# Kernel optimization log

Measured on AMD Instinct MI355X. Metric: run time of the kernel, lower is better.

Reference implementation:

```python
import jax, jax.numpy as jnp
import numpy as np

B, S, D, H = 4, 2048, 1024, 16
DK = D // H
FF = 2 * D


def _layer_norm(x, g, b, eps):
    mu = jnp.mean(x, axis=-1, keepdims=True)
    var = jnp.mean(jnp.square(x - mu), axis=-1, keepdims=True)
    return (x - mu) * jax.lax.rsqrt(var + eps) * g + b


def setup_inputs() -> dict:
    key = jax.random.key(0)
    ks = jax.random.split(key, 8)
    s = 1.0 / np.sqrt(D)
    return {
        "x": jax.random.normal(ks[0], (B, S, D), jnp.float32),
        "Wq": jax.random.normal(ks[1], (D, D), jnp.float32) * s,
        "Wk": jax.random.normal(ks[2], (D, D), jnp.float32) * s,
        "Wv": jax.random.normal(ks[3], (D, D), jnp.float32) * s,
        "Wo": jax.random.normal(ks[4], (D, D), jnp.float32) * s,
        "ln1_g": jnp.ones((D,), jnp.float32),
        "ln1_b": jnp.zeros((D,), jnp.float32),
        "fc1_w": jax.random.normal(ks[5], (D, FF), jnp.float32) * s,
        "fc1_b": jnp.zeros((FF,), jnp.float32),
        "fc2_w": jax.random.normal(ks[6], (FF, D), jnp.float32) * (1.0 / np.sqrt(FF)),
        "fc2_b": jnp.zeros((D,), jnp.float32),
        "ln2_g": jnp.ones((D,), jnp.float32),
        "ln2_b": jnp.zeros((D,), jnp.float32),
    }


def reference(x, Wq, Wk, Wv, Wo, ln1_g, ln1_b, fc1_w, fc1_b, fc2_w, fc2_b, ln2_g, ln2_b):
    # --- multi-head self-attention (pre-LN, residual) ---
    residual = x
    xn = _layer_norm(x, ln1_g, ln1_b, 1e-5)  # nn.LayerNorm default eps
    q = (xn @ Wq).reshape(B, S, H, DK)
    k = (xn @ Wk).reshape(B, S, H, DK)
    v = (xn @ Wv).reshape(B, S, H, DK)
    scores = jnp.einsum("bqhd,bkhd->bhqk", q, k) / jnp.sqrt(jnp.float32(DK))
    attn = jax.nn.softmax(scores, axis=-1)  # dropout p=0.0 -> identity
    out = jnp.einsum("bhqk,bkhd->bqhd", attn, v).reshape(B, S, D)
    out = out @ Wo + residual
    # --- residual feed-forward (pre-LN, eps=1e-6) ---
    h = _layer_norm(out, ln2_g, ln2_b, 1e-6)
    h = jax.nn.relu(h @ fc1_w + fc1_b)
    h = h @ fc2_w + fc2_b
    return out + h
```

## Files before the change

kernel.cpp:

```cpp
#include <hip/hip_runtime.h>

#define BB   4
#define SS   2048
#define DDIM 1024
#define HH   16
#define DKK  64
#define FFF  2048
#define NTOK (BB * SS)

typedef __bf16 bf16x8 __attribute__((ext_vector_type(8)));
typedef float floatx4 __attribute__((ext_vector_type(4)));

__device__ __forceinline__ unsigned short f2bf(float f) {
    union { float f; unsigned u; } v; v.f = f;
    unsigned r = v.u + 0x7fffu + ((v.u >> 16) & 1u);
    return (unsigned short)(r >> 16);
}

__device__ __forceinline__ void async_copy16(const unsigned short* g, unsigned short* l) {
    __builtin_amdgcn_global_load_lds(
        (const __attribute__((address_space(1))) void*)g,
        (__attribute__((address_space(3))) void*)l, 16, 0, 0);
}

__device__ __forceinline__ unsigned pack_bf_trunc(float a, float b) {
    union { float f; unsigned u; } x, y; x.f = a; y.f = b;
    return __builtin_amdgcn_perm(y.u, x.u, 0x07060302u);
}

__global__ __launch_bounds__(256) void transpose_all(
    const float* __restrict__ Wq, const float* __restrict__ Wk,
    const float* __restrict__ Wv, const float* __restrict__ Wo,
    const float* __restrict__ fc1, const float* __restrict__ fc2,
    unsigned short* __restrict__ wqkT, unsigned short* __restrict__ wvT,
    unsigned short* __restrict__ woT, unsigned short* __restrict__ fc1T,
    unsigned short* __restrict__ fc2T) {
    __shared__ float tile[64][65];
    int t = blockIdx.x;
    const float* src; unsigned short* dst; int K, N, tl;
    if (t < 256)       { src = Wq;  dst = wqkT;                       K = 1024; N = 1024; tl = t; }
    else if (t < 512)  { src = Wk;  dst = wqkT + (size_t)1024 * 1024; K = 1024; N = 1024; tl = t - 256; }
    else if (t < 768)  { src = Wv;  dst = wvT;                        K = 1024; N = 1024; tl = t - 512; }
    else if (t < 1024) { src = Wo;  dst = woT;                        K = 1024; N = 1024; tl = t - 768; }
    else if (t < 1536) { src = fc1; dst = fc1T;                       K = 1024; N = 2048; tl = t - 1024; }
    else               { src = fc2; dst = fc2T;                       K = 2048; N = 1024; tl = t - 1536; }
    int kt = K >> 6;
    int k0 = (tl & (kt - 1)) * 64, n0 = (tl / kt) * 64;
    int tid = threadIdx.x;
#pragma unroll
    for (int i = 0; i < 16; ++i) {
        int e = i * 256 + tid;
        int r = e >> 6, c = e & 63;
        tile[r][c] = src[(size_t)(k0 + r) * N + (n0 + c)];
    }
    __syncthreads();
#pragma unroll
    for (int i = 0; i < 16; ++i) {
        int e = i * 256 + tid;
        int r = e >> 6, c = e & 63;
        dst[(size_t)(n0 + r) * K + (k0 + c)] = f2bf(tile[c][r]);
    }
}

__device__ __forceinline__ float block_sum256(float s) {
#pragma unroll
    for (int o = 32; o > 0; o >>= 1) s += __shfl_xor(s, o);
    __shared__ float partial[4];
    int w = threadIdx.x >> 6;
    __syncthreads();
    if ((threadIdx.x & 63) == 0) partial[w] = s;
    __syncthreads();
    return partial[0] + partial[1] + partial[2] + partial[3];
}

__global__ __launch_bounds__(256) void layernorm_bf16(
    const float* __restrict__ x, const float* __restrict__ g,
    const float* __restrict__ b, unsigned short* __restrict__ out, float eps) {
    size_t row = blockIdx.x;
    const float* xr = x + row * DDIM;
    int tid = threadIdx.x;
    float4 v = *(const float4*)(xr + tid * 4);
    float mu = block_sum256(v.x + v.y + v.z + v.w) * (1.0f / DDIM);
    float dx = v.x - mu, dy = v.y - mu, dz = v.z - mu, dw = v.w - mu;
    float var = block_sum256(dx * dx + dy * dy + dz * dz + dw * dw) * (1.0f / DDIM);
    float rstd = rsqrtf(var + eps);
    int c = tid * 4;
    unsigned short* o = out + row * DDIM + c;
    o[0] = f2bf(dx * rstd * g[c + 0] + b[c + 0]);
    o[1] = f2bf(dy * rstd * g[c + 1] + b[c + 1]);
    o[2] = f2bf(dz * rstd * g[c + 2] + b[c + 2]);
    o[3] = f2bf(dw * rstd * g[c + 3] + b[c + 3]);
}

__global__ __launch_bounds__(256) void gemm_bt128(
    const unsigned short* __restrict__ A, const unsigned short* __restrict__ Bt,
    const float* __restrict__ bias, const float* __restrict__ resid,
    float* __restrict__ outf, unsigned short* __restrict__ outh,
    int M, int N, int K, int relu) {
    __shared__ unsigned short As[128 * 64];
    __shared__ unsigned short Bs[128 * 64];
    int tid = threadIdx.x;
    int wave = tid >> 6, lane = tid & 63;
    int lr = lane & 15, quad = lane >> 4;
    int bid = blockIdx.x;
    int m0 = (bid & 63) * 128;
    int n0 = (bid >> 6) * 128;
    int wm = (wave >> 1) * 64, wn = (wave & 1) * 64;

    floatx4 acc[4][4];
#pragma unroll
    for (int i = 0; i < 4; ++i)
#pragma unroll
        for (int t = 0; t < 4; ++t)
#pragma unroll
            for (int r = 0; r < 4; ++r) acc[i][t][r] = 0.0f;

    int srow = 32 * wave + (lane >> 3);
    int scol = (lane & 7) * 8;
    const unsigned short* ag[4];
    const unsigned short* bg[4];
    unsigned short* al[4];
    unsigned short* bl[4];
#pragma unroll
    for (int c = 0; c < 4; ++c) {
        ag[c] = A  + (size_t)(m0 + srow + 8 * c) * K + scol;
        bg[c] = Bt + (size_t)(n0 + srow + 8 * c) * K + scol;
        al[c] = &As[(32 * wave + 8 * c) * 64];
        bl[c] = &Bs[(32 * wave + 8 * c) * 64];
    }

    for (int k0 = 0; k0 < K; k0 += 64) {
#pragma unroll
        for (int c = 0; c < 4; ++c) {
            async_copy16(ag[c] + k0, al[c]);
            async_copy16(bg[c] + k0, bl[c]);
        }
        __syncthreads();
#pragma unroll
        for (int kk = 0; kk < 2; ++kk) {
            bf16x8 af[4], bfr[4];
#pragma unroll
            for (int i = 0; i < 4; ++i)
                af[i] = *(const bf16x8*)&As[(wm + 16 * i + lr) * 64 + kk * 32 + quad * 8];
#pragma unroll
            for (int t = 0; t < 4; ++t)
                bfr[t] = *(const bf16x8*)&Bs[(wn + 16 * t + lr) * 64 + kk * 32 + quad * 8];
#pragma unroll
            for (int i = 0; i < 4; ++i)
#pragma unroll
                for (int t = 0; t < 4; ++t)
                    acc[i][t] = __builtin_amdgcn_mfma_f32_16x16x32_bf16(af[i], bfr[t], acc[i][t], 0, 0, 0);
        }
        __syncthreads();
    }

#pragma unroll
    for (int i = 0; i < 4; ++i) {
#pragma unroll
        for (int t = 0; t < 4; ++t) {
            int col = n0 + wn + 16 * t + lr;
#pragma unroll
            for (int r = 0; r < 4; ++r) {
                int row = m0 + wm + 16 * i + quad * 4 + r;
                float v = acc[i][t][r];
                if (bias)  v += bias[col];
                if (resid) v += resid[(size_t)row * N + col];
                if (relu)  v = fmaxf(v, 0.0f);
                size_t idx = (size_t)row * N + col;
                if (outf) outf[idx] = v;
                else      outh[idx] = f2bf(v);
            }
        }
    }
}

__global__ __launch_bounds__(256) void transpose_v(
    const unsigned short* __restrict__ vb, unsigned short* __restrict__ vt) {
    int bh = blockIdx.y;
    int b = bh >> 4, h = bh & 15;
    int s = blockIdx.x * 256 + threadIdx.x;
    size_t inbase = ((size_t)(b * SS + s)) * DDIM + h * 64;
    size_t outbase = (size_t)bh * 64 * SS;
    int sp = (s & ~63) + 4 * (s & 15) + ((s >> 4) & 3);
#pragma unroll
    for (int dk8 = 0; dk8 < 8; ++dk8) {
        uint4 raw = *(const uint4*)(vb + inbase + dk8 * 8);
        const unsigned short* ph = (const unsigned short*)&raw;
#pragma unroll
        for (int i = 0; i < 8; ++i)
            vt[outbase + (size_t)(dk8 * 8 + i) * SS + sp] = ph[i];
    }
}

#define AST 72
#define VST 136

__global__ __launch_bounds__(256, 2) void attention_mfma4(
    const unsigned short* __restrict__ qk, const unsigned short* __restrict__ vt,
    unsigned short* __restrict__ ctx) {
    __shared__ unsigned short Qs[128 * AST];
    __shared__ unsigned short Ks[128 * AST];
    __shared__ unsigned short Vs[64 * VST];
    __shared__ unsigned short Ps[128 * AST];

    int tid = threadIdx.x;
    int wave = tid >> 6, lane = tid & 63;
    int lr = lane & 15, quad = lane >> 4;

    int bid = blockIdx.x;
    int bh = bid & 63;
    int qt = bid >> 6;
    int b = bh >> 4, h = bh & 15;
    int q0 = qt * 128;
    size_t q_base = ((size_t)b * SS) * 2048 + h * 64;
    size_t k_base = q_base + 1024;
    size_t vt_base = (size_t)bh * 64 * SS;

#pragma unroll
    for (int i = 0; i < 4; ++i) {
        int e = i * 256 + tid;
        int r = e >> 3, c8 = (e & 7) * 8;
        *(uint4*)&Qs[r * AST + c8] =
            *(const uint4*)(qk + q_base + (size_t)(q0 + r) * 2048 + c8);
    }

    floatx4 o[2][4];
    float l[2][4];
#pragma unroll
    for (int g = 0; g < 2; ++g)
#pragma unroll
        for (int t = 0; t < 4; ++t)
#pragma unroll
            for (int r = 0; r < 4; ++r) o[g][t][r] = 0.0f;
#pragma unroll
    for (int g = 0; g < 2; ++g)
#pragma unroll
        for (int r = 0; r < 4; ++r) l[g][r] = 0.0f;

    const float C = 0.18033688011112042f;

    for (int jt = 0; jt < SS / 128; ++jt) {
#pragma unroll
        for (int i = 0; i < 4; ++i) {
            int e = i * 256 + tid;
            int r = e >> 3, c8 = (e & 7) * 8;
            *(uint4*)&Ks[r * AST + c8] =
                *(const uint4*)(qk + k_base + (size_t)(jt * 128 + r) * 2048 + c8);
        }
#pragma unroll
        for (int i = 0; i < 4; ++i) {
            int e = i * 256 + tid;
            int r = e >> 4, c8 = (e & 15) * 8;
            *(uint4*)&Vs[r * VST + c8] =
                *(const uint4*)(vt + vt_base + (size_t)r * SS + jt * 128 + c8);
        }
        __syncthreads();

        floatx4 s[2][8];
#pragma unroll
        for (int g = 0; g < 2; ++g)
#pragma unroll
            for (int t = 0; t < 8; ++t)
#pragma unroll
                for (int r = 0; r < 4; ++r) s[g][t][r] = 0.0f;
#pragma unroll
        for (int kk = 0; kk < 2; ++kk) {
            bf16x8 af0 = *(const bf16x8*)&Qs[(32 * wave + lr) * AST + kk * 32 + quad * 8];
            bf16x8 af1 = *(const bf16x8*)&Qs[(32 * wave + 16 + lr) * AST + kk * 32 + quad * 8];
#pragma unroll
            for (int t = 0; t < 8; ++t) {
                bf16x8 bfr = *(const bf16x8*)&Ks[(16 * t + lr) * AST + kk * 32 + quad * 8];
                s[0][t] = __builtin_amdgcn_mfma_f32_16x16x32_bf16(af0, bfr, s[0][t], 0, 0, 0);
                s[1][t] = __builtin_amdgcn_mfma_f32_16x16x32_bf16(af1, bfr, s[1][t], 0, 0, 0);
            }
        }

        uint2 pw1[2][4];
#pragma unroll
        for (int g = 0; g < 2; ++g) {
#pragma unroll
            for (int r = 0; r < 4; ++r) {
                float p[8];
#pragma unroll
                for (int t = 0; t < 8; ++t) p[t] = exp2f(s[g][t][r] * C);
                l[g][r] += ((p[0] + p[1]) + (p[2] + p[3])) + ((p[4] + p[5]) + (p[6] + p[7]));
                uint2 w0;
                w0.x = pack_bf_trunc(p[0], p[1]);
                w0.y = pack_bf_trunc(p[2], p[3]);
                *(uint2*)&Ps[(32 * wave + 16 * g + quad * 4 + r) * AST + 4 * lr] = w0;
                pw1[g][r].x = pack_bf_trunc(p[4], p[5]);
                pw1[g][r].y = pack_bf_trunc(p[6], p[7]);
            }
        }

#pragma unroll
        for (int kk = 0; kk < 2; ++kk) {
            bf16x8 pf0 = *(const bf16x8*)&Ps[(32 * wave + lr) * AST + kk * 32 + quad * 8];
            bf16x8 pf1 = *(const bf16x8*)&Ps[(32 * wave + 16 + lr) * AST + kk * 32 + quad * 8];
#pragma unroll
            for (int t = 0; t < 4; ++t) {
                bf16x8 vf = *(const bf16x8*)&Vs[(16 * t + lr) * VST + kk * 32 + quad * 8];
                o[0][t] = __builtin_amdgcn_mfma_f32_16x16x32_bf16(pf0, vf, o[0][t], 0, 0, 0);
                o[1][t] = __builtin_amdgcn_mfma_f32_16x16x32_bf16(pf1, vf, o[1][t], 0, 0, 0);
            }
        }
#pragma unroll
        for (int g = 0; g < 2; ++g)
#pragma unroll
            for (int r = 0; r < 4; ++r)
                *(uint2*)&Ps[(32 * wave + 16 * g + quad * 4 + r) * AST + 4 * lr] = pw1[g][r];
#pragma unroll
        for (int kk = 0; kk < 2; ++kk) {
            bf16x8 pf0 = *(const bf16x8*)&Ps[(32 * wave + lr) * AST + kk * 32 + quad * 8];
            bf16x8 pf1 = *(const bf16x8*)&Ps[(32 * wave + 16 + lr) * AST + kk * 32 + quad * 8];
#pragma unroll
            for (int t = 0; t < 4; ++t) {
                bf16x8 vf = *(const bf16x8*)&Vs[(16 * t + lr) * VST + 64 + kk * 32 + quad * 8];
                o[0][t] = __builtin_amdgcn_mfma_f32_16x16x32_bf16(pf0, vf, o[0][t], 0, 0, 0);
                o[1][t] = __builtin_amdgcn_mfma_f32_16x16x32_bf16(pf1, vf, o[1][t], 0, 0, 0);
            }
        }
        __syncthreads();
    }

#pragma unroll
    for (int g = 0; g < 2; ++g) {
#pragma unroll
        for (int r = 0; r < 4; ++r) {
            float ls = l[g][r];
            ls += __shfl_xor(ls, 1);
            ls += __shfl_xor(ls, 2);
            ls += __shfl_xor(ls, 4);
            ls += __shfl_xor(ls, 8);
            float inv = 1.0f / ls;
            int row = q0 + 32 * wave + 16 * g + quad * 4 + r;
            size_t base = ((size_t)(b * SS + row)) * DDIM + h * 64;
#pragma unroll
            for (int t = 0; t < 4; ++t)
                ctx[base + 16 * t + lr] = f2bf(o[g][t][r] * inv);
        }
    }
}

extern "C" void kernel_launch(void* const* d_in, const int* in_sizes, int n_in,
                              void* d_out, int out_size, void* d_ws, size_t ws_size,
                              hipStream_t stream) {
    const float* x     = (const float*)d_in[0];
    const float* Wq    = (const float*)d_in[1];
    const float* Wk    = (const float*)d_in[2];
    const float* Wv    = (const float*)d_in[3];
    const float* Wo    = (const float*)d_in[4];
    const float* ln1g  = (const float*)d_in[5];
    const float* ln1b  = (const float*)d_in[6];
    const float* fc1w  = (const float*)d_in[7];
    const float* fc1b  = (const float*)d_in[8];
    const float* fc2w  = (const float*)d_in[9];
    const float* fc2b  = (const float*)d_in[10];
    const float* ln2g  = (const float*)d_in[11];
    const float* ln2b  = (const float*)d_in[12];
    float* out = (float*)d_out;

    char* ws = (char*)d_ws;
    const size_t MB = 1024 * 1024;
    unsigned short* wqkT = (unsigned short*)(ws + 0 * MB);
    unsigned short* wvT  = (unsigned short*)(ws + 4 * MB);
    unsigned short* woT  = (unsigned short*)(ws + 6 * MB);
    unsigned short* fc1T = (unsigned short*)(ws + 8 * MB);
    unsigned short* fc2T = (unsigned short*)(ws + 12 * MB);
    unsigned short* xn   = (unsigned short*)(ws + 16 * MB);
    unsigned short* vt   = xn;
    unsigned short* hn   = xn;
    unsigned short* qkb  = (unsigned short*)(ws + 32 * MB);
    unsigned short* h1   = qkb;
    unsigned short* vb   = (unsigned short*)(ws + 64 * MB);
    unsigned short* ctx  = vb;

    dim3 blk(256);

    transpose_all<<<2048, blk, 0, stream>>>(Wq, Wk, Wv, Wo, fc1w, fc2w,
                                            wqkT, wvT, woT, fc1T, fc2T);

    layernorm_bf16<<<NTOK, blk, 0, stream>>>(x, ln1g, ln1b, xn, 1e-5f);

    gemm_bt128<<<1024, blk, 0, stream>>>(xn, wqkT, nullptr, nullptr, nullptr, qkb, NTOK, 2048, 1024, 0);
    gemm_bt128<<<512, blk, 0, stream>>>(xn, wvT, nullptr, nullptr, nullptr, vb, NTOK, 1024, 1024, 0);
    transpose_v<<<dim3(8, 64), blk, 0, stream>>>(vb, vt);

    attention_mfma4<<<1024, blk, 0, stream>>>(qkb, vt, ctx);

    gemm_bt128<<<512, blk, 0, stream>>>(ctx, woT, nullptr, x, out, nullptr, NTOK, 1024, 1024, 0);
    layernorm_bf16<<<NTOK, blk, 0, stream>>>(out, ln2g, ln2b, hn, 1e-6f);
    gemm_bt128<<<1024, blk, 0, stream>>>(hn, fc1T, fc1b, nullptr, nullptr, h1, NTOK, 2048, 1024, 1);
    gemm_bt128<<<512, blk, 0, stream>>>(h1, fc2T, fc2b, out, out, nullptr, NTOK, 1024, 2048, 0);
}
```

Measured before the change: 579.8 us.

## Load MFMA fragments directly from global memory in GEMM and attention

The GEMM drops LDS staging and async copies: each wave loads its A/B MFMA fragments straight from global memory into registers, with no block barriers. Attention is restructured so waves split the key range in two halves, keep Q fragments in registers, and read K and transposed V directly from global memory. Partial outputs and row sums are combined through LDS at the end. This removes LDS traffic and syncs, but gives up cross-wave reuse inside a block, so it relies on cache hits and adds more global load instructions.

```diff
diff --git a/kernel.cpp b/kernel.cpp
--- a/kernel.cpp
+++ b/kernel.cpp
@@ -17,15 +17,13 @@
     return (unsigned short)(r >> 16);
 }
 
-__device__ __forceinline__ void async_copy16(const unsigned short* g, unsigned short* l) {
-    __builtin_amdgcn_global_load_lds(
-        (const __attribute__((address_space(1))) void*)g,
-        (__attribute__((address_space(3))) void*)l, 16, 0, 0);
-}
-
 __device__ __forceinline__ unsigned pack_bf_trunc(float a, float b) {
     union { float f; unsigned u; } x, y; x.f = a; y.f = b;
     return __builtin_amdgcn_perm(y.u, x.u, 0x07060302u);
+}
+
+__device__ __forceinline__ bf16x8 as_frag(uint4 v) {
+    union { uint4 u; bf16x8 f; } c; c.u = v; return c.f;
 }
 
 __global__ __launch_bounds__(256) void transpose_all(
@@ -92,13 +90,11 @@
     o[3] = f2bf(dw * rstd * g[c + 3] + b[c + 3]);
 }
 
-__global__ __launch_bounds__(256) void gemm_bt128(
+__global__ __launch_bounds__(256, 2) void gemm_reg(
     const unsigned short* __restrict__ A, const unsigned short* __restrict__ Bt,
     const float* __restrict__ bias, const float* __restrict__ resid,
     float* __restrict__ outf, unsigned short* __restrict__ outh,
     int M, int N, int K, int relu) {
-    __shared__ unsigned short As[128 * 64];
-    __shared__ unsigned short Bs[128 * 64];
     int tid = threadIdx.x;
     int wave = tid >> 6, lane = tid & 63;
     int lr = lane & 15, quad = lane >> 4;
@@ -115,43 +111,22 @@
 #pragma unroll
             for (int r = 0; r < 4; ++r) acc[i][t][r] = 0.0f;
 
-    int srow = 32 * wave + (lane >> 3);
-    int scol = (lane & 7) * 8;
-    const unsigned short* ag[4];
-    const unsigned short* bg[4];
-    unsigned short* al[4];
-    unsigned short* bl[4];
-#pragma unroll
-    for (int c = 0; c < 4; ++c) {
-        ag[c] = A  + (size_t)(m0 + srow + 8 * c) * K + scol;
-        bg[c] = Bt + (size_t)(n0 + srow + 8 * c) * K + scol;
-        al[c] = &As[(32 * wave + 8 * c) * 64];
-        bl[c] = &Bs[(32 * wave + 8 * c) * 64];
-    }
-
-    for (int k0 = 0; k0 < K; k0 += 64) {
-#pragma unroll
-        for (int c = 0; c < 4; ++c) {
-            async_copy16(ag[c] + k0, al[c]);
-            async_copy16(bg[c] + k0, bl[c]);
-        }
-        __syncthreads();
-#pragma unroll
-        for (int kk = 0; kk < 2; ++kk) {
-            bf16x8 af[4], bfr[4];
-#pragma unroll
-            for (int i = 0; i < 4; ++i)
-                af[i] = *(const bf16x8*)&As[(wm + 16 * i + lr) * 64 + kk * 32 + quad * 8];
+    const unsigned short* ap = A  + (size_t)(m0 + wm + lr) * K + quad * 8;
+    const unsigned short* bp = Bt + (size_t)(n0 + wn + lr) * K + quad * 8;
+
+    for (int k0 = 0; k0 < K; k0 += 32) {
+        uint4 av[4], bv[4];
+#pragma unroll
+        for (int i = 0; i < 4; ++i) {
+            av[i] = *(const uint4*)(ap + (size_t)(16 * i) * K + k0);
+            bv[i] = *(const uint4*)(bp + (size_t)(16 * i) * K + k0);
+        }
+#pragma unroll
+        for (int i = 0; i < 4; ++i)
 #pragma unroll
             for (int t = 0; t < 4; ++t)
-                bfr[t] = *(const bf16x8*)&Bs[(wn + 16 * t + lr) * 64 + kk * 32 + quad * 8];
-#pragma unroll
-            for (int i = 0; i < 4; ++i)
-#pragma unroll
-                for (int t = 0; t < 4; ++t)
-                    acc[i][t] = __builtin_amdgcn_mfma_f32_16x16x32_bf16(af[i], bfr[t], acc[i][t], 0, 0, 0);
-        }
-        __syncthreads();
+                acc[i][t] = __builtin_amdgcn_mfma_f32_16x16x32_bf16(
+                    as_frag(av[i]), as_frag(bv[t]), acc[i][t], 0, 0, 0);
     }
 
 #pragma unroll
@@ -192,20 +167,17 @@
     }
 }
 
-#define AST 72
-#define VST 136
-
-__global__ __launch_bounds__(256, 2) void attention_mfma4(
+#define PST 68
+
+__global__ __launch_bounds__(256, 2) void attention_mfma5(
     const unsigned short* __restrict__ qk, const unsigned short* __restrict__ vt,
     unsigned short* __restrict__ ctx) {
-    __shared__ unsigned short Qs[128 * AST];
-    __shared__ unsigned short Ks[128 * AST];
-    __shared__ unsigned short Vs[64 * VST];
-    __shared__ unsigned short Ps[128 * AST];
+    __shared__ unsigned short Ps[256 * PST];
 
     int tid = threadIdx.x;
     int wave = tid >> 6, lane = tid & 63;
     int lr = lane & 15, quad = lane >> 4;
+    int wq = wave >> 1, wj = wave & 1;
 
     int bid = blockIdx.x;
     int bh = bid & 63;
@@ -216,129 +188,131 @@
     size_t k_base = q_base + 1024;
     size_t vt_base = (size_t)bh * 64 * SS;
 
-#pragma unroll
-    for (int i = 0; i < 4; ++i) {
-        int e = i * 256 + tid;
-        int r = e >> 3, c8 = (e & 7) * 8;
-        *(uint4*)&Qs[r * AST + c8] =
-            *(const uint4*)(qk + q_base + (size_t)(q0 + r) * 2048 + c8);
-    }
-
-    floatx4 o[2][4];
-    float l[2][4];
-#pragma unroll
-    for (int g = 0; g < 2; ++g)
-#pragma unroll
-        for (int t = 0; t < 4; ++t)
-#pragma unroll
-            for (int r = 0; r < 4; ++r) o[g][t][r] = 0.0f;
-#pragma unroll
-    for (int g = 0; g < 2; ++g)
-#pragma unroll
-        for (int r = 0; r < 4; ++r) l[g][r] = 0.0f;
-
+    uint4 af[4][2];
+#pragma unroll
+    for (int i = 0; i < 4; ++i)
+#pragma unroll
+        for (int kk = 0; kk < 2; ++kk)
+            af[i][kk] = *(const uint4*)(qk + q_base +
+                (size_t)(q0 + 64 * wq + 16 * i + lr) * 2048 + kk * 32 + quad * 8);
+
+    floatx4 o[4][4];
+    float l[4][4];
+#pragma unroll
+    for (int i = 0; i < 4; ++i)
+#pragma unroll
+        for (int t = 0; t < 4; ++t) {
+#pragma unroll
+            for (int r = 0; r < 4; ++r) o[i][t][r] = 0.0f;
+            l[i][t] = 0.0f;
+        }
+
+    unsigned short* myPs = &Ps[wave * 64 * PST];
     const float C = 0.18033688011112042f;
 
     for (int jt = 0; jt < SS / 128; ++jt) {
+        int j0 = jt * 128 + 64 * wj;
+
+        floatx4 s[4][4];
+#pragma unroll
+        for (int i = 0; i < 4; ++i)
+#pragma unroll
+            for (int t = 0; t < 4; ++t)
+#pragma unroll
+                for (int r = 0; r < 4; ++r) s[i][t][r] = 0.0f;
+#pragma unroll
+        for (int kk = 0; kk < 2; ++kk) {
+            uint4 bv[4];
+#pragma unroll
+            for (int t = 0; t < 4; ++t)
+                bv[t] = *(const uint4*)(qk + k_base +
+                    (size_t)(j0 + 16 * t + lr) * 2048 + kk * 32 + quad * 8);
+#pragma unroll
+            for (int i = 0; i < 4; ++i)
+#pragma unroll
+                for (int t = 0; t < 4; ++t)
+                    s[i][t] = __builtin_amdgcn_mfma_f32_16x16x32_bf16(
+                        as_frag(af[i][kk]), as_frag(bv[t]), s[i][t], 0, 0, 0);
+        }
+
 #pragma unroll
         for (int i = 0; i < 4; ++i) {
-            int e = i * 256 + tid;
-            int r = e >> 3, c8 = (e & 7) * 8;
-            *(uint4*)&Ks[r * AST + c8] =
-                *(const uint4*)(qk + k_base + (size_t)(jt * 128 + r) * 2048 + c8);
-        }
-#pragma unroll
-        for (int i = 0; i < 4; ++i) {
-            int e = i * 256 + tid;
-            int r = e >> 4, c8 = (e & 15) * 8;
-            *(uint4*)&Vs[r * VST + c8] =
-                *(const uint4*)(vt + vt_base + (size_t)r * SS + jt * 128 + c8);
-        }
-        __syncthreads();
-
-        floatx4 s[2][8];
-#pragma unroll
-        for (int g = 0; g < 2; ++g)
-#pragma unroll
-            for (int t = 0; t < 8; ++t)
-#pragma unroll
-                for (int r = 0; r < 4; ++r) s[g][t][r] = 0.0f;
+#pragma unroll
+            for (int r = 0; r < 4; ++r) {
+                float p0 = exp2f(s[i][0][r] * C);
+                float p1 = exp2f(s[i][1][r] * C);
+                float p2 = exp2f(s[i][2][r] * C);
+                float p3 = exp2f(s[i][3][r] * C);
+                l[i][r] += (p0 + p1) + (p2 + p3);
+                uint2 w;
+                w.x = pack_bf_trunc(p0, p1);
+                w.y = pack_bf_trunc(p2, p3);
+                *(uint2*)&myPs[(16 * i + quad * 4 + r) * PST + 4 * lr] = w;
+            }
+        }
+
 #pragma unroll
         for (int kk = 0; kk < 2; ++kk) {
-            bf16x8 af0 = *(const bf16x8*)&Qs[(32 * wave + lr) * AST + kk * 32 + quad * 8];
-            bf16x8 af1 = *(const bf16x8*)&Qs[(32 * wave + 16 + lr) * AST + kk * 32 + quad * 8];
-#pragma unroll
-            for (int t = 0; t < 8; ++t) {
-                bf16x8 bfr = *(const bf16x8*)&Ks[(16 * t + lr) * AST + kk * 32 + quad * 8];
-                s[0][t] = __builtin_amdgcn_mfma_f32_16x16x32_bf16(af0, bfr, s[0][t], 0, 0, 0);
-                s[1][t] = __builtin_amdgcn_mfma_f32_16x16x32_bf16(af1, bfr, s[1][t], 0, 0, 0);
-            }
-        }
-
-        uint2 pw1[2][4];
-#pragma unroll
-        for (int g = 0; g < 2; ++g) {
-#pragma unroll
-            for (int r = 0; r < 4; ++r) {
-                float p[8];
-#pragma unroll
-                for (int t = 0; t < 8; ++t) p[t] = exp2f(s[g][t][r] * C);
-                l[g][r] += ((p[0] + p[1]) + (p[2] + p[3])) + ((p[4] + p[5]) + (p[6] + p[7]));
-                uint2 w0;
-                w0.x = pack_bf_trunc(p[0], p[1]);
-                w0.y = pack_bf_trunc(p[2], p[3]);
-                *(uint2*)&Ps[(32 * wave + 16 * g + quad * 4 + r) * AST + 4 * lr] = w0;
-                pw1[g][r].x = pack_bf_trunc(p[4], p[5]);
-                pw1[g][r].y = pack_bf_trunc(p[6], p[7]);
-            }
-        }
-
-#pragma unroll
-        for (int kk = 0; kk < 2; ++kk) {
-            bf16x8 pf0 = *(const bf16x8*)&Ps[(32 * wave + lr) * AST + kk * 32 + quad * 8];
-            bf16x8 pf1 = *(const bf16x8*)&Ps[(32 * wave + 16 + lr) * AST + kk * 32 + quad * 8];
-#pragma unroll
-            for (int t = 0; t < 4; ++t) {
-                bf16x8 vf = *(const bf16x8*)&Vs[(16 * t + lr) * VST + kk * 32 + quad * 8];
-                o[0][t] = __builtin_amdgcn_mfma_f32_16x16x32_bf16(pf0, vf, o[0][t], 0, 0, 0);
-                o[1][t] = __builtin_amdgcn_mfma_f32_16x16x32_bf16(pf1, vf, o[1][t], 0, 0, 0);
-            }
-        }
-#pragma unroll
-        for (int g = 0; g < 2; ++g)
-#pragma unroll
-            for (int r = 0; r < 4; ++r)
-                *(uint2*)&Ps[(32 * wave + 16 * g + quad * 4 + r) * AST + 4 * lr] = pw1[g][r];
-#pragma unroll
-        for (int kk = 0; kk < 2; ++kk) {
-            bf16x8 pf0 = *(const bf16x8*)&Ps[(32 * wave + lr) * AST + kk * 32 + quad * 8];
-            bf16x8 pf1 = *(const bf16x8*)&Ps[(32 * wave + 16 + lr) * AST + kk * 32 + quad * 8];
-#pragma unroll
-            for (int t = 0; t < 4; ++t) {
-                bf16x8 vf = *(const bf16x8*)&Vs[(16 * t + lr) * VST + 64 + kk * 32 + quad * 8];
-                o[0][t] = __builtin_amdgcn_mfma_f32_16x16x32_bf16(pf0, vf, o[0][t], 0, 0, 0);
-                o[1][t] = __builtin_amdgcn_mfma_f32_16x16x32_bf16(pf1, vf, o[1][t], 0, 0, 0);
-            }
-        }
-        __syncthreads();
-    }
-
-#pragma unroll
-    for (int g = 0; g < 2; ++g) {
+            uint4 vv[4];
+#pragma unroll
+            for (int t = 0; t < 4; ++t)
+                vv[t] = *(const uint4*)(vt + vt_base +
+                    (size_t)(16 * t + lr) * SS + j0 + kk * 32 + quad * 8);
+            bf16x8 pf[4];
+#pragma unroll
+            for (int i = 0; i < 4; ++i)
+                pf[i] = *(const bf16x8*)&myPs[(16 * i + lr) * PST + kk * 32 + quad * 8];
+#pragma unroll
+            for (int i = 0; i < 4; ++i)
+#pragma unroll
+                for (int t = 0; t < 4; ++t)
+                    o[i][t] = __builtin_amdgcn_mfma_f32_16x16x32_bf16(
+                        pf[i], as_frag(vv[t]), o[i][t], 0, 0, 0);
+        }
+    }
+
+#pragma unroll
+    for (int i = 0; i < 4; ++i)
 #pragma unroll
         for (int r = 0; r < 4; ++r) {
-            float ls = l[g][r];
+            float ls = l[i][r];
             ls += __shfl_xor(ls, 1);
             ls += __shfl_xor(ls, 2);
             ls += __shfl_xor(ls, 4);
             ls += __shfl_xor(ls, 8);
-            float inv = 1.0f / ls;
-            int row = q0 + 32 * wave + 16 * g + quad * 4 + r;
-            size_t base = ((size_t)(b * SS + row)) * DDIM + h * 64;
-#pragma unroll
-            for (int t = 0; t < 4; ++t)
-                ctx[base + 16 * t + lr] = f2bf(o[g][t][r] * inv);
-        }
+            l[i][r] = ls;
+        }
+
+    __syncthreads();
+    float* obuf = (float*)Ps;
+    float* lbuf = obuf + 2 * 64 * 65;
+    if (wj == 1) {
+#pragma unroll
+        for (int i = 0; i < 4; ++i)
+#pragma unroll
+            for (int r = 0; r < 4; ++r) {
+                int rl = 16 * i + quad * 4 + r;
+#pragma unroll
+                for (int t = 0; t < 4; ++t)
+                    obuf[(wq * 64 + rl) * 65 + 16 * t + lr] = o[i][t][r];
+                if (lr == 0) lbuf[wq * 64 + rl] = l[i][r];
+            }
+    }
+    __syncthreads();
+    if (wj == 0) {
+#pragma unroll
+        for (int i = 0; i < 4; ++i)
+#pragma unroll
+            for (int r = 0; r < 4; ++r) {
+                int rl = 16 * i + quad * 4 + r;
+                float inv = 1.0f / (l[i][r] + lbuf[wq * 64 + rl]);
+                int row = q0 + 64 * wq + rl;
+                size_t base = ((size_t)(b * SS + row)) * DDIM + h * 64;
+#pragma unroll
+                for (int t = 0; t < 4; ++t)
+                    ctx[base + 16 * t + lr] =
+                        f2bf((o[i][t][r] + obuf[(wq * 64 + rl) * 65 + 16 * t + lr]) * inv);
+            }
     }
 }
 
@@ -382,14 +356,14 @@
 
     layernorm_bf16<<<NTOK, blk, 0, stream>>>(x, ln1g, ln1b, xn, 1e-5f);
 
-    gemm_bt128<<<1024, blk, 0, stream>>>(xn, wqkT, nullptr, nullptr, nullptr, qkb, NTOK, 2048, 1024, 0);
-    gemm_bt128<<<512, blk, 0, stream>>>(xn, wvT, nullptr, nullptr, nullptr, vb, NTOK, 1024, 1024, 0);
+    gemm_reg<<<1024, blk, 0, stream>>>(xn, wqkT, nullptr, nullptr, nullptr, qkb, NTOK, 2048, 1024, 0);
+    gemm_reg<<<512, blk, 0, stream>>>(xn, wvT, nullptr, nullptr, nullptr, vb, NTOK, 1024, 1024, 0);
     transpose_v<<<dim3(8, 64), blk, 0, stream>>>(vb, vt);
 
-    attention_mfma4<<<1024, blk, 0, stream>>>(qkb, vt, ctx);
-
-    gemm_bt128<<<512, blk, 0, stream>>>(ctx, woT, nullptr, x, out, nullptr, NTOK, 1024, 1024, 0);
+    attention_mfma5<<<1024, blk, 0, stream>>>(qkb, vt, ctx);
+
+    gemm_reg<<<512, blk, 0, stream>>>(ctx, woT, nullptr, x, out, nullptr, NTOK, 1024, 1024, 0);
     layernorm_bf16<<<NTOK, blk, 0, stream>>>(out, ln2g, ln2b, hn, 1e-6f);
-    gemm_bt128<<<1024, blk, 0, stream>>>(hn, fc1T, fc1b, nullptr, nullptr, h1, NTOK, 2048, 1024, 1);
-    gemm_bt128<<<512, blk, 0, stream>>>(h1, fc2T, fc2b, out, out, nullptr, NTOK, 1024, 2048, 0);
-}
+    gemm_reg<<<1024, blk, 0, stream>>>(hn, fc1T, fc1b, nullptr, nullptr, h1, NTOK, 2048, 1024, 1);
+    gemm_reg<<<512, blk, 0, stream>>>(h1, fc2T, fc2b, out, out, nullptr, NTOK, 1024, 2048, 0);
+}
```

New measurement: 829.5 us. 1.43x slower.
